# Kernel optimization log

Hardware: AMD Instinct MI355X
Metric: run time of the kernel (lower is better)

## Reference

```python
import jax, jax.numpy as jnp
import numpy as np

B, L, E, H, Dff = 2, 2048, 1024, 16, 4096
Dh = E // H


def _ln(x, g, b, eps=1e-5):
    m = jnp.mean(x, axis=-1, keepdims=True)
    v = jnp.mean((x - m) ** 2, axis=-1, keepdims=True)
    return (x - m) / jnp.sqrt(v + eps) * g + b


def setup_inputs() -> dict:
    key = jax.random.key(0)
    ks = jax.random.split(key, 16)
    s_e = 1.0 / np.sqrt(E)
    s_d = 1.0 / np.sqrt(Dff)
    inp = {
        "x": jax.random.normal(ks[0], (B, L, E), jnp.float32),
        # causal mask: positions with 0 are masked out (masked_fill(mask==0, -1e9))
        "mask": jnp.tril(jnp.ones((L, L), jnp.bool_)),
        # per-head QKV projections, stacked over heads: (H, E, Dh), biases (H, Dh)
        "Wq": jax.random.uniform(ks[1], (H, E, Dh), jnp.float32, -s_e, s_e),
        "bq": jax.random.uniform(ks[2], (H, Dh), jnp.float32, -s_e, s_e),
        "Wk": jax.random.uniform(ks[3], (H, E, Dh), jnp.float32, -s_e, s_e),
        "bk": jax.random.uniform(ks[4], (H, Dh), jnp.float32, -s_e, s_e),
        "Wv": jax.random.uniform(ks[5], (H, E, Dh), jnp.float32, -s_e, s_e),
        "bv": jax.random.uniform(ks[6], (H, Dh), jnp.float32, -s_e, s_e),
        "Wo": jax.random.uniform(ks[7], (E, E), jnp.float32, -s_e, s_e),
        "bo": jax.random.uniform(ks[8], (E,), jnp.float32, -s_e, s_e),
        "W1": jax.random.uniform(ks[9], (E, Dff), jnp.float32, -s_e, s_e),
        "c1": jax.random.uniform(ks[10], (Dff,), jnp.float32, -s_e, s_e),
        "W2": jax.random.uniform(ks[11], (Dff, E), jnp.float32, -s_d, s_d),
        "c2": jax.random.uniform(ks[12], (E,), jnp.float32, -s_d, s_d),
        "g1": jnp.ones((E,), jnp.float32),
        "beta1": jnp.zeros((E,), jnp.float32),
        "g2": jnp.ones((E,), jnp.float32),
        "beta2": jnp.zeros((E,), jnp.float32),
    }
    return inp


def reference(x, mask, Wq, bq, Wk, bk, Wv, bv, Wo, bo, W1, c1, W2, c2, g1, beta1, g2, beta2):
    # Batched equivalent of the per-head Attention loop (eval mode: dropout = identity)
    q = jnp.einsum("ble,hed->bhld", x, Wq) + bq[None, :, None, :]
    k = jnp.einsum("ble,hed->bhld", x, Wk) + bk[None, :, None, :]
    v = jnp.einsum("ble,hed->bhld", x, Wv) + bv[None, :, None, :]
    scores = jnp.einsum("bhld,bhmd->bhlm", q, k) / np.sqrt(Dh).astype(np.float32)
    scores = jnp.where(mask[None, None, :, :], scores, -1e9)
    p = jax.nn.softmax(scores, axis=-1)
    z = jnp.einsum("bhlm,bhmd->bhld", p, v)  # (B,H,L,Dh)
    z = z.transpose(0, 2, 1, 3).reshape(B, L, E)  # concat heads
    att = z @ Wo + bo
    h = _ln(x + att, g1, beta1)
    ff = jax.nn.relu(h @ W1 + c1) @ W2 + c2
    out = _ln(h + ff, g2, beta2)
    return out
```

## Files before the change

kernel.cpp:

```cpp
#include <hip/hip_runtime.h>
#include <hip/hip_bf16.h>
#include <math.h>

#define B_   2
#define L_   2048
#define E_   1024
#define H_   16
#define DH   64
#define DFF  4096
#define M_   4096
#define APAD 72
#define SCALE_Q 0.18033688011112042f

typedef __attribute__((ext_vector_type(8))) short short8;
typedef __attribute__((ext_vector_type(4))) float f32x4;
typedef __bf16 bf16x8 __attribute__((ext_vector_type(8)));

__device__ __forceinline__ float bf2f(unsigned short u) {
    return __uint_as_float(((unsigned)u) << 16);
}
__device__ __forceinline__ unsigned short f2bf(float f) {
    unsigned u = __float_as_uint(f);
    return (unsigned short)((u + 0x7fff + ((u >> 16) & 1)) >> 16);
}
__device__ __forceinline__ unsigned pk_trunc(float lo, float hi) {
    return (__float_as_uint(lo) >> 16) | (__float_as_uint(hi) & 0xffff0000u);
}

__device__ __forceinline__ void gld16(const unsigned short* g, unsigned short* l) {
    __builtin_amdgcn_global_load_lds(
        (const __attribute__((address_space(1))) void*)g,
        (__attribute__((address_space(3))) void*)l, 16, 0, 0);
}

__global__ __launch_bounds__(256) void prep(const float* __restrict__ x,
                                            const float* __restrict__ Wq,
                                            const float* __restrict__ Wk,
                                            const float* __restrict__ Wv,
                                            const float* __restrict__ bq,
                                            const float* __restrict__ bk,
                                            const float* __restrict__ bv,
                                            const float* __restrict__ Wo,
                                            const float* __restrict__ W1,
                                            const float* __restrict__ W2,
                                            unsigned short* __restrict__ xb,
                                            unsigned short* __restrict__ Wqkvt,
                                            unsigned short* __restrict__ Wot,
                                            unsigned short* __restrict__ W1t,
                                            unsigned short* __restrict__ W2t,
                                            float* __restrict__ bqkv) {
    __shared__ float tile[32][33];
    int bid = blockIdx.x;
    const int t = threadIdx.x;

    if (bid < 4096) {
        int i = (bid * 256 + t) * 4;
        float4 v = *(const float4*)&x[i];
        ushort4 pk = { f2bf(v.x), f2bf(v.y), f2bf(v.z), f2bf(v.w) };
        *(ushort4*)&xb[i] = pk;
        return;
    }
    bid -= 4096;

    const float* in; unsigned short* outp; int R, C, r0, c0; float sc = 1.f;
    if (bid < 3072) {
        int xq = bid & 1, yq = (bid >> 1) & 31, wh = bid >> 6;
        int which = wh >> 4, h = wh & 15;
        in   = (which == 0 ? Wq : which == 1 ? Wk : Wv) + (size_t)h * E_ * DH;
        outp = Wqkvt + ((size_t)which * 1024 + h * 64) * 1024;
        R = E_; C = DH; r0 = yq * 32; c0 = xq * 32;
        if (which == 0) sc = SCALE_Q;
    } else if (bid < 4096) {
        bid -= 3072;
        in = Wo; outp = Wot; R = E_; C = E_;
        c0 = (bid & 31) * 32; r0 = (bid >> 5) * 32;
    } else if (bid < 8192) {
        bid -= 4096;
        in = W1; outp = W1t; R = E_; C = DFF;
        c0 = (bid & 127) * 32; r0 = (bid >> 7) * 32;
    } else if (bid < 12288) {
        bid -= 8192;
        in = W2; outp = W2t; R = DFF; C = E_;
        c0 = (bid & 31) * 32; r0 = (bid >> 5) * 32;
    } else {
        bid -= 12288;
        int n = bid * 256 + t;
        bqkv[n] = n < 1024 ? bq[n] * SCALE_Q : n < 2048 ? bk[n - 1024] : bv[n - 2048];
        return;
    }

    const int tx = t & 31, tq = t >> 5;
#pragma unroll
    for (int s2 = 0; s2 < 4; s2++)
        tile[tq * 4 + s2][tx] = in[(size_t)(r0 + tq * 4 + s2) * C + c0 + tx] * sc;
    __syncthreads();
    const int cc = t >> 3, rq = (t & 7) * 4;
    ushort4 pk = { f2bf(tile[rq + 0][cc]), f2bf(tile[rq + 1][cc]),
                   f2bf(tile[rq + 2][cc]), f2bf(tile[rq + 3][cc]) };
    *(ushort4*)&outp[(size_t)(c0 + cc) * R + r0 + rq] = pk;
}

__global__ __launch_bounds__(256) void v_transpose_perm(const unsigned short* __restrict__ qkv,
                                                        unsigned short* __restrict__ vtg) {
    __shared__ unsigned short tile[64 * APAD];
    const int t  = threadIdx.x;
    const int kt = blockIdx.x, hh = blockIdx.y, b = blockIdx.z;
    const int rr0 = t >> 3, o8 = (t & 7) * 8, rr1 = rr0 + 32;
    const size_t gbase = ((size_t)b * L_ + kt * 64) * 3072 + 2048 + hh * 64;
    *(short8*)&tile[rr0 * APAD + o8] = *(const short8*)&qkv[gbase + (size_t)rr0 * 3072 + o8];
    *(short8*)&tile[rr1 * APAD + o8] = *(const short8*)&qkv[gbase + (size_t)rr1 * 3072 + o8];
    __syncthreads();
    const size_t obase = ((size_t)(b * H_ + hh) * 64) * (size_t)L_ + kt * 64;
    const int a = t & 15, d0 = (t >> 4) * 4;
#pragma unroll
    for (int s2 = 0; s2 < 4; s2++) {
        int d = d0 + s2;
        ushort4 pk = { tile[(a +  0) * APAD + d], tile[(a + 16) * APAD + d],
                       tile[(a + 32) * APAD + d], tile[(a + 48) * APAD + d] };
        *(ushort4*)&vtg[obase + (size_t)d * L_ + 4 * a] = pk;
    }
}

#define BAR() __builtin_amdgcn_s_barrier()
#define PIN() __builtin_amdgcn_sched_barrier(0)

#define RD_A(DST, BB, QR) do {                                                \
    _Pragma("unroll") for (int mi = 0; mi < 4; mi++)                          \
    _Pragma("unroll") for (int ks = 0; ks < 2; ks++)                          \
        DST[mi][ks] = *(const bf16x8*)&As[(BB) * 16384 + ((QR) * 128 + aRow + mi * 16) * 64 + (ks ? cs1 : cs0)]; \
} while (0)

#define RD_B(DST, BB, QC) do {                                                \
    _Pragma("unroll") for (int nj = 0; nj < 2; nj++)                          \
    _Pragma("unroll") for (int ks = 0; ks < 2; ks++)                          \
        DST[nj][ks] = *(const bf16x8*)&Bs[(BB) * 16384 + ((QC) * 128 + bRow + nj * 16) * 64 + (ks ? cs1 : cs0)]; \
} while (0)

#define MM(QR, QC, AF, BF) do {                                               \
    __builtin_amdgcn_s_setprio(1);                                            \
    _Pragma("unroll") for (int mi = 0; mi < 4; mi++)                          \
    _Pragma("unroll") for (int nj = 0; nj < 2; nj++)                          \
    _Pragma("unroll") for (int ks = 0; ks < 2; ks++)                          \
        acc[QR][QC][mi][nj] = __builtin_amdgcn_mfma_f32_16x16x32_bf16(        \
            AF[mi][ks], BF[nj][ks], acc[QR][QC][mi][nj], 0, 0, 0);            \
    __builtin_amdgcn_s_setprio(0);                                            \
} while (0)

template <int RELU, int SK>
__global__ __launch_bounds__(512, 2) void gemm256(const unsigned short* __restrict__ A,
                                                  const unsigned short* __restrict__ Bt,
                                                  const float* __restrict__ bias,
                                                  unsigned short* __restrict__ P0,
                                                  unsigned short* __restrict__ P1,
                                                  unsigned short* __restrict__ P2,
                                                  unsigned short* __restrict__ P3,
                                                  int M, int N, int K) {
    extern __shared__ __align__(16) unsigned short g_lds[];
    unsigned short* As = g_lds;
    unsigned short* Bs = g_lds + 32768;

    const int t    = threadIdx.x;
    const int lane = t & 63;
    const int w    = t >> 6;
    const int quad = lane >> 4;
    const int l16  = lane & 15;

    const int lin = blockIdx.x;
    const int xcd = lin & 7, s = lin >> 3;
    int m0, n0, kbeg, KT;
    unsigned short* C;
    if (SK) {
        m0 = ((xcd << 1) | (s & 1)) * 256;
        const int rest = s >> 1;
        n0 = (rest & 3) * 256;
        const int z  = rest >> 2;
        const int K4 = K >> 2;
        kbeg = z * K4;
        KT   = K4 >> 6;
        C = (z == 0) ? P0 : (z == 1) ? P1 : (z == 2) ? P2 : P3;
    } else {
        const int NT2 = (N >> 8) >> 1;
        m0 = (((xcd & 3) << 2) | (s & 3)) * 256;
        n0 = ((xcd >> 2) * NT2 + (s >> 2)) * 256;
        kbeg = 0;
        KT   = K >> 6;
        C = P0;
    }

    const int srow = t >> 3;
    const int ksw  = ((t & 7) ^ (srow & 7)) * 8;
    const size_t aStage = (size_t)(m0 + srow) * K + kbeg + ksw;
    const size_t bStage = (size_t)(n0 + srow) * K + kbeg + ksw;

    auto stageA = [&](int buf, int h, int v) {
        size_t g = aStage + (size_t)(h * 128) * K + (size_t)v * 64;
        unsigned short* l = As + buf * 16384 + h * 8192 + w * 512;
        gld16(A + g, l);
        gld16(A + g + (size_t)64 * K, l + 4096);
    };
    auto stageB = [&](int buf, int h, int v) {
        size_t g = bStage + (size_t)(h * 128) * K + (size_t)v * 64;
        unsigned short* l = Bs + buf * 16384 + h * 8192 + w * 512;
        gld16(Bt + g, l);
        gld16(Bt + g + (size_t)64 * K, l + 4096);
    };

    const int aRow = (w >> 2) * 64 + l16;
    const int bRow = (w & 3) * 32 + l16;
    const int cs0  = (quad ^ (l16 & 7)) * 8;
    const int cs1  = cs0 ^ 32;

    f32x4 acc[2][2][4][2];
#pragma unroll
    for (int a1i = 0; a1i < 2; a1i++)
#pragma unroll
        for (int a2 = 0; a2 < 2; a2++)
#pragma unroll
            for (int a3 = 0; a3 < 4; a3++)
#pragma unroll
                for (int a4 = 0; a4 < 2; a4++)
                    acc[a1i][a2][a3][a4] = (f32x4){0.f, 0.f, 0.f, 0.f};

    bf16x8 a0[4][2], a1[4][2], b0[2][2], b1[2][2];

    stageA(0, 0, 0); stageB(0, 0, 0); stageA(0, 1, 0); stageB(0, 1, 0);
    if (KT > 1) {
        stageA(1, 0, 1); stageB(1, 0, 1);
        asm volatile("s_waitcnt vmcnt(4)" ::: "memory");
    } else {
        asm volatile("s_waitcnt vmcnt(0)" ::: "memory");
    }
    BAR();
    RD_A(a0, 0, 0);
    RD_B(b0, 0, 0);
    PIN();

    for (int u = 0; u < KT; ++u) {
        const int bb = u & 1;
        const int nb = bb ^ 1;

        RD_B(b1, bb, 1);
        if (u + 1 < KT) stageB(nb, 1, u + 1);
        PIN();
        BAR();
        MM(0, 0, a0, b0);
        BAR();

        RD_A(a1, bb, 1);
        if (u + 1 < KT) stageA(nb, 1, u + 1);
        PIN();
        BAR();
        MM(0, 1, a0, b1);
        BAR();

        if (u + 2 < KT) stageA(bb, 0, u + 2);
        PIN();
        BAR();
        MM(1, 0, a1, b0);
        BAR();

        if (u + 2 < KT) {
            stageB(bb, 0, u + 2);
            asm volatile("s_waitcnt vmcnt(4)" ::: "memory");
        } else if (u + 1 < KT) {
            asm volatile("s_waitcnt vmcnt(0)" ::: "memory");
        }
        PIN();
        BAR();
        if (u + 1 < KT) {
            RD_A(a0, nb, 0);
            RD_B(b0, nb, 0);
            PIN();
        }
        MM(1, 1, a1, b1);
        BAR();
    }

#pragma unroll
    for (int qr = 0; qr < 2; qr++)
#pragma unroll
        for (int qc = 0; qc < 2; qc++)
#pragma unroll
            for (int nj = 0; nj < 2; nj++) {
                const int col = n0 + qc * 128 + (w & 3) * 32 + nj * 16 + l16;
                const float bv = SK ? 0.f : bias[col];
#pragma unroll
                for (int mi = 0; mi < 4; mi++) {
                    const int row = m0 + qr * 128 + (w >> 2) * 64 + mi * 16 + quad * 4;
#pragma unroll
                    for (int r = 0; r < 4; r++) {
                        float v = acc[qr][qc][mi][nj][r] + bv;
                        if (RELU) v = fmaxf(v, 0.f);
                        C[(size_t)(row + r) * N + col] = f2bf(v);
                    }
                }
            }
}

__global__ __launch_bounds__(256, 2) void attn_mfma(const unsigned short* __restrict__ qkv,
                                                    const unsigned short* __restrict__ vtg,
                                                    unsigned short* __restrict__ oA,
                                                    unsigned short* __restrict__ oB,
                                                    float* __restrict__ lA,
                                                    float* __restrict__ lB) {
    __shared__ __align__(16) unsigned short ks[2][64 * APAD];
    __shared__ __align__(16) unsigned short vt[64 * APAD];
    __shared__ __align__(16) unsigned short ps[128 * APAD];

    const int t    = threadIdx.x;
    const int lane = t & 63;
    const int w    = t >> 6;
    const int l16  = lane & 15;
    const int quad = lane >> 4;

    const int lin  = blockIdx.x;
    const int unit = lin >> 8;
    const int l8   = lin & 255;
    const int xcd  = l8 & 7;
    const int s    = l8 >> 3;
    const int hh   = xcd * 2 + (s & 1);
    const int rest = s >> 1;
    const int b    = rest & 1;
    const int pair = rest >> 1;

    unsigned short* __restrict__ oP = unit ? oB : oA;
    float* __restrict__ lP = unit ? lB : lA;

    const size_t rowbase = (size_t)b * L_;
    const size_t vbase   = ((size_t)(b * H_ + hh) * 64) * (size_t)L_;
    const int rr0 = t >> 3, o8 = (t & 7) * 8, rr1 = rr0 + 32;

    for (int ph = 0; ph < 2; ph++) {
        const int qq = ph ? pair : 15 - pair;
        const int cnt = qq + 1;

        bf16x8 qf[2][2];
#pragma unroll
        for (int g = 0; g < 2; g++) {
            size_t qrow = rowbase + qq * 128 + w * 32 + g * 16 + l16;
#pragma unroll
            for (int c = 0; c < 2; c++)
                qf[g][c] = *(const bf16x8*)&qkv[qrow * 3072 + hh * 64 + c * 32 + quad * 8];
        }

        f32x4 o[2][4];
#pragma unroll
        for (int g = 0; g < 2; g++)
#pragma unroll
            for (int j = 0; j < 4; j++) o[g][j] = (f32x4){0.f, 0.f, 0.f, 0.f};
        float l_i[2][4] = {};

        {
            size_t kg = (rowbase + unit * 64) * 3072 + 1024 + hh * 64;
            short8 k0 = *(const short8*)&qkv[kg + (size_t)rr0 * 3072 + o8];
            short8 k1 = *(const short8*)&qkv[kg + (size_t)rr1 * 3072 + o8];
            short8 v0 = *(const short8*)&vtg[vbase + unit * 64 + (size_t)rr0 * L_ + o8];
            short8 v1 = *(const short8*)&vtg[vbase + unit * 64 + (size_t)rr1 * L_ + o8];
            *(short8*)&ks[0][rr0 * APAD + o8] = k0;
            *(short8*)&ks[0][rr1 * APAD + o8] = k1;
            *(short8*)&vt[rr0 * APAD + o8] = v0;
            *(short8*)&vt[rr1 * APAD + o8] = v1;
        }

        short8 k0a, k0b, v0a, v0b, k1a, k1b, v1a, v1b;
        if (cnt > 1) {
            const int kt1 = unit + 2;
            size_t kg = (rowbase + kt1 * 64) * 3072 + 1024 + hh * 64;
            k1a = *(const short8*)&qkv[kg + (size_t)rr0 * 3072 + o8];
            k1b = *(const short8*)&qkv[kg + (size_t)rr1 * 3072 + o8];
            size_t vg = vbase + kt1 * 64;
            v1a = *(const short8*)&vtg[vg + (size_t)rr0 * L_ + o8];
            v1b = *(const short8*)&vtg[vg + (size_t)rr1 * L_ + o8];
        }

        auto tile_body = [&](int i,
                             short8& ika, short8& ikb, short8& iva, short8& ivb,
                             short8& wka, short8& wkb, short8& wva, short8& wvb) {
            const int kt = unit + 2 * i;
            const int p  = i & 1;
            __syncthreads();

            if (i + 2 < cnt) {
                size_t kg = (rowbase + (kt + 4) * 64) * 3072 + 1024 + hh * 64;
                ika = *(const short8*)&qkv[kg + (size_t)rr0 * 3072 + o8];
                ikb = *(const short8*)&qkv[kg + (size_t)rr1 * 3072 + o8];
                size_t vg = vbase + (kt + 4) * 64;
                iva = *(const short8*)&vtg[vg + (size_t)rr0 * L_ + o8];
                ivb = *(const short8*)&vtg[vg + (size_t)rr1 * L_ + o8];
            }

            f32x4 s4[2][4];
#pragma unroll
            for (int g = 0; g < 2; g++)
#pragma unroll
                for (int j = 0; j < 4; j++) s4[g][j] = (f32x4){0.f, 0.f, 0.f, 0.f};
            __builtin_amdgcn_s_setprio(1);
#pragma unroll
            for (int c = 0; c < 2; c++)
#pragma unroll
                for (int j = 0; j < 4; j++) {
                    bf16x8 kf = *(const bf16x8*)&ks[p][(j * 16 + l16) * APAD + c * 32 + quad * 8];
#pragma unroll
                    for (int g = 0; g < 2; g++)
                        s4[g][j] = __builtin_amdgcn_mfma_f32_16x16x32_bf16(qf[g][c], kf, s4[g][j], 0, 0, 0);
                }
            __builtin_amdgcn_s_setprio(0);

            if (kt >= 2 * qq) {
#pragma unroll
                for (int g = 0; g < 2; g++)
#pragma unroll
                    for (int j = 0; j < 4; j++) {
                        int lk = kt * 64 + j * 16 + l16;
#pragma unroll
                        for (int r = 0; r < 4; r++)
                            if (lk > qq * 128 + w * 32 + g * 16 + quad * 4 + r)
                                s4[g][j][r] = -INFINITY;
                    }
            }

#pragma unroll
            for (int g = 0; g < 2; g++)
#pragma unroll
                for (int r = 0; r < 4; r++) {
                    float p0 = __builtin_amdgcn_exp2f(s4[g][0][r]);
                    float p1 = __builtin_amdgcn_exp2f(s4[g][1][r]);
                    float p2 = __builtin_amdgcn_exp2f(s4[g][2][r]);
                    float p3 = __builtin_amdgcn_exp2f(s4[g][3][r]);
                    l_i[g][r] += (p0 + p1) + (p2 + p3);
                    uint2 pk = { pk_trunc(p0, p1), pk_trunc(p2, p3) };
                    *(uint2*)&ps[(w * 32 + g * 16 + quad * 4 + r) * APAD + 4 * l16] = pk;
                }

            __builtin_amdgcn_s_waitcnt(0xc07f);

            __builtin_amdgcn_s_setprio(1);
#pragma unroll
            for (int c = 0; c < 2; c++) {
                bf16x8 pf[2];
#pragma unroll
                for (int g = 0; g < 2; g++)
                    pf[g] = *(const bf16x8*)&ps[(w * 32 + g * 16 + l16) * APAD + c * 32 + quad * 8];
#pragma unroll
                for (int j = 0; j < 4; j++) {
                    bf16x8 vf = *(const bf16x8*)&vt[(j * 16 + l16) * APAD + c * 32 + quad * 8];
#pragma unroll
                    for (int g = 0; g < 2; g++)
                        o[g][j] = __builtin_amdgcn_mfma_f32_16x16x32_bf16(pf[g], vf, o[g][j], 0, 0, 0);
                }
            }
            __builtin_amdgcn_s_setprio(0);

            __syncthreads();
            if (i + 1 < cnt) {
                *(short8*)&ks[p ^ 1][rr0 * APAD + o8] = wka;
                *(short8*)&ks[p ^ 1][rr1 * APAD + o8] = wkb;
                *(short8*)&vt[rr0 * APAD + o8] = wva;
                *(short8*)&vt[rr1 * APAD + o8] = wvb;
            }
        };

        for (int i = 0; i < cnt; i += 2) {
            tile_body(i,     k0a, k0b, v0a, v0b, k1a, k1b, v1a, v1b);
            if (i + 1 < cnt)
                tile_body(i + 1, k1a, k1b, v1a, v1b, k0a, k0b, v0a, v0b);
        }

#pragma unroll
        for (int g = 0; g < 2; g++)
#pragma unroll
            for (int r = 0; r < 4; r++) {
                float l = l_i[g][r];
                l += __shfl_xor(l, 1);
                l += __shfl_xor(l, 2);
                l += __shfl_xor(l, 4);
                l += __shfl_xor(l, 8);
                int rowq = qq * 128 + w * 32 + g * 16 + quad * 4 + r;
                size_t grow = (size_t)(b * H_ + hh) * L_ + rowq;
                if (l16 == 0) lP[grow] = l;
#pragma unroll
                for (int j = 0; j < 4; j++)
                    oP[grow * 64 + j * 16 + l16] = f2bf(o[g][j][r]);
            }
    }
}

__global__ __launch_bounds__(256) void attn_combine(const unsigned short* __restrict__ oA,
                                                    const unsigned short* __restrict__ oB,
                                                    const float* __restrict__ lA,
                                                    const float* __restrict__ lB,
                                                    unsigned short* __restrict__ zb) {
    const int t = threadIdx.x;
    const size_t idx4 = ((size_t)blockIdx.x * 256 + t) * 4;
    const size_t row  = idx4 >> 6;
    const int    col  = (int)(idx4 & 63);

    float inv = 1.f / (lA[row] + lB[row]);
    ushort4 ua = *(const ushort4*)&oA[idx4];
    ushort4 ub = *(const ushort4*)&oB[idx4];

    const int bq   = (int)(row >> 15);
    const int hh   = (int)((row >> 11) & 15);
    const int rowq = (int)(row & 2047);
    size_t z = ((size_t)(bq * L_ + rowq)) * 1024 + hh * 64 + col;
    ushort4 pk = { f2bf((bf2f(ua.x) + bf2f(ub.x)) * inv),
                   f2bf((bf2f(ua.y) + bf2f(ub.y)) * inv),
                   f2bf((bf2f(ua.z) + bf2f(ub.z)) * inv),
                   f2bf((bf2f(ua.w) + bf2f(ub.w)) * inv) };
    *(ushort4*)&zb[z] = pk;
}

template <int WRITE_BF16>
__global__ __launch_bounds__(256) void ln5_kernel(const float* __restrict__ a,
                                                  const unsigned short* __restrict__ q0,
                                                  const unsigned short* __restrict__ q1,
                                                  const unsigned short* __restrict__ q2,
                                                  const unsigned short* __restrict__ q3,
                                                  const float* __restrict__ bias,
                                                  const float* __restrict__ g,
                                                  const float* __restrict__ be,
                                                  float* __restrict__ out,
                                                  unsigned short* __restrict__ out_bf) {
    __shared__ float s1[256], s2[256];
    const int row = blockIdx.x;
    const int t   = threadIdx.x;
    const size_t base = (size_t)row * E_ + t * 4;

    float4 ya = *(const float4*)&a[base];
    ushort4 u0 = *(const ushort4*)&q0[base];
    ushort4 u1 = *(const ushort4*)&q1[base];
    ushort4 u2 = *(const ushort4*)&q2[base];
    ushort4 u3 = *(const ushort4*)&q3[base];
    float4 bb = *(const float4*)&bias[t * 4];
    float y0 = ya.x + bb.x + bf2f(u0.x) + bf2f(u1.x) + bf2f(u2.x) + bf2f(u3.x);
    float y1 = ya.y + bb.y + bf2f(u0.y) + bf2f(u1.y) + bf2f(u2.y) + bf2f(u3.y);
    float y2 = ya.z + bb.z + bf2f(u0.z) + bf2f(u1.z) + bf2f(u2.z) + bf2f(u3.z);
    float y3 = ya.w + bb.w + bf2f(u0.w) + bf2f(u1.w) + bf2f(u2.w) + bf2f(u3.w);

    s1[t] = y0 + y1 + y2 + y3;
    s2[t] = y0 * y0 + y1 * y1 + y2 * y2 + y3 * y3;
    __syncthreads();
    for (int off = 128; off > 0; off >>= 1) {
        if (t < off) { s1[t] += s1[t + off]; s2[t] += s2[t + off]; }
        __syncthreads();
    }
    float mean = s1[0] * (1.0f / E_);
    float var  = s2[0] * (1.0f / E_) - mean * mean;
    float rstd = rsqrtf(var + 1e-5f);

    float4 gv = *(const float4*)&g[t * 4];
    float4 bv = *(const float4*)&be[t * 4];
    float4 ov;
    ov.x = (y0 - mean) * rstd * gv.x + bv.x;
    ov.y = (y1 - mean) * rstd * gv.y + bv.y;
    ov.z = (y2 - mean) * rstd * gv.z + bv.z;
    ov.w = (y3 - mean) * rstd * gv.w + bv.w;
    *(float4*)&out[base] = ov;
    if (WRITE_BF16) {
        ushort4 pk = { f2bf(ov.x), f2bf(ov.y), f2bf(ov.z), f2bf(ov.w) };
        *(ushort4*)&out_bf[base] = pk;
    }
}

extern "C" void kernel_launch(void* const* d_in, const int* in_sizes, int n_in,
                              void* d_out, int out_size, void* d_ws, size_t ws_size,
                              hipStream_t stream)
{
    const float* x     = (const float*)d_in[0];
    const float* Wq    = (const float*)d_in[2];
    const float* bq    = (const float*)d_in[3];
    const float* Wk    = (const float*)d_in[4];
    const float* bk    = (const float*)d_in[5];
    const float* Wv    = (const float*)d_in[6];
    const float* bv    = (const float*)d_in[7];
    const float* Wo    = (const float*)d_in[8];
    const float* bo    = (const float*)d_in[9];
    const float* W1    = (const float*)d_in[10];
    const float* c1    = (const float*)d_in[11];
    const float* W2    = (const float*)d_in[12];
    const float* c2    = (const float*)d_in[13];
    const float* g1    = (const float*)d_in[14];
    const float* beta1 = (const float*)d_in[15];
    const float* g2    = (const float*)d_in[16];
    const float* beta2 = (const float*)d_in[17];
    float* out = (float*)d_out;

    const size_t MB = 1024 * 1024;
    char* w = (char*)d_ws;
    unsigned short* xb    = (unsigned short*)(w + 0 * MB);
    unsigned short* Wqkvt = (unsigned short*)(w + 8 * MB);
    unsigned short* Wot   = (unsigned short*)(w + 14 * MB);
    unsigned short* W1t   = (unsigned short*)(w + 16 * MB);
    unsigned short* W2t   = (unsigned short*)(w + 24 * MB);
    float*          bqkv  = (float*)(w + 32 * MB);
    unsigned short* qkv   = (unsigned short*)(w + 33 * MB);
    float*          h     = (float*)(w + 65 * MB);
    unsigned short* vtg   = (unsigned short*)(w + 89 * MB);
    unsigned short* oPA   = (unsigned short*)(w + 57 * MB);
    unsigned short* oPB   = (unsigned short*)(w + 81 * MB);
    float*          lPA   = (float*)(w + 32 * MB);
    float*          lPB   = (float*)(w + 32 * MB + 262144);
    unsigned short* zb    = (unsigned short*)(w + 0 * MB);
    unsigned short* ap0   = (unsigned short*)(w + 33 * MB);
    unsigned short* ap1   = (unsigned short*)(w + 41 * MB);
    unsigned short* ap2   = (unsigned short*)(w + 49 * MB);
    unsigned short* ap3   = (unsigned short*)(w + 89 * MB);
    unsigned short* hb    = (unsigned short*)(w + 0 * MB);
    unsigned short* ff1b  = (unsigned short*)(w + 33 * MB);
    unsigned short* fp0   = (unsigned short*)(w + 0 * MB);
    unsigned short* fp1   = (unsigned short*)(w + 8 * MB);
    unsigned short* fp2   = (unsigned short*)(w + 16 * MB);
    unsigned short* fp3   = (unsigned short*)(w + 81 * MB);

    static bool lds_inited = false;
    if (!lds_inited) {
        (void)hipFuncSetAttribute((const void*)&gemm256<0, 0>,
                                  hipFuncAttributeMaxDynamicSharedMemorySize, 131072);
        (void)hipFuncSetAttribute((const void*)&gemm256<1, 0>,
                                  hipFuncAttributeMaxDynamicSharedMemorySize, 131072);
        (void)hipFuncSetAttribute((const void*)&gemm256<0, 1>,
                                  hipFuncAttributeMaxDynamicSharedMemorySize, 131072);
        lds_inited = true;
    }

    dim3 blk(256);
    dim3 blk2(512);

    prep<<<dim3(16396), blk, 0, stream>>>(x, Wq, Wk, Wv, bq, bk, bv, Wo, W1, W2,
                                          xb, Wqkvt, Wot, W1t, W2t, bqkv);

    gemm256<0, 0><<<dim3(192), blk2, 131072, stream>>>(xb, Wqkvt, bqkv,
                                                       qkv, nullptr, nullptr, nullptr,
                                                       M_, 3072, E_);

    v_transpose_perm<<<dim3(L_ / 64, H_, B_), blk, 0, stream>>>(qkv, vtg);

    attn_mfma<<<dim3(512), blk, 0, stream>>>(qkv, vtg, oPA, oPB, lPA, lPB);

    attn_combine<<<dim3(4096), blk, 0, stream>>>(oPA, oPB, lPA, lPB, zb);

    gemm256<0, 1><<<dim3(256), blk2, 131072, stream>>>(zb, Wot, nullptr,
                                                       ap0, ap1, ap2, ap3,
                                                       M_, E_, E_);

    ln5_kernel<1><<<dim3(M_), blk, 0, stream>>>(x, ap0, ap1, ap2, ap3, bo, g1, beta1, h, hb);

    gemm256<1, 0><<<dim3(256), blk2, 131072, stream>>>(hb, W1t, c1,
                                                       ff1b, nullptr, nullptr, nullptr,
                                                       M_, DFF, E_);

    gemm256<0, 1><<<dim3(256), blk2, 131072, stream>>>(ff1b, W2t, nullptr,
                                                       fp0, fp1, fp2, fp3,
                                                       M_, E_, DFF);

    ln5_kernel<0><<<dim3(M_), blk, 0, stream>>>(h, fp0, fp1, fp2, fp3, c2, g2, beta2, out, nullptr);
}
```

Before: 333.9 us.

## Fuse attention split-combine into the output-projection GEMM A-tile staging

Removes the separate attn_combine kernel and instead has the Wo split-K GEMM build its A tiles by loading both partial attention outputs and their row sums, normalizing, and writing bf16 into LDS. This drops one launch and the write and re-read of the combined z buffer. In exchange, A staging now goes through registers rather than direct global-to-LDS loads, with extra waitcnt on LDS writes, which may weaken the software pipeline. Each split-K block does a single 64-wide head slice per k-step.

```diff
diff --git a/kernel.cpp b/kernel.cpp
--- a/kernel.cpp
+++ b/kernel.cpp
@@ -31,6 +31,16 @@
     __builtin_amdgcn_global_load_lds(
         (const __attribute__((address_space(1))) void*)g,
         (__attribute__((address_space(3))) void*)l, 16, 0, 0);
+}
+
+__device__ __forceinline__ short8 comb8(short8 a, short8 b, float inv) {
+    short8 r;
+#pragma unroll
+    for (int i = 0; i < 8; i++) {
+        float v = (bf2f((unsigned short)a[i]) + bf2f((unsigned short)b[i])) * inv;
+        r[i] = (short)f2bf(v);
+    }
+    return r;
 }
 
 __global__ __launch_bounds__(256) void prep(const float* __restrict__ x,
@@ -146,7 +156,7 @@
     __builtin_amdgcn_s_setprio(0);                                            \
 } while (0)
 
-template <int RELU, int SK>
+template <int RELU, int SK, int COMB>
 __global__ __launch_bounds__(512, 2) void gemm256(const unsigned short* __restrict__ A,
                                                   const unsigned short* __restrict__ Bt,
                                                   const float* __restrict__ bias,
@@ -154,6 +164,10 @@
                                                   unsigned short* __restrict__ P1,
                                                   unsigned short* __restrict__ P2,
                                                   unsigned short* __restrict__ P3,
+                                                  const unsigned short* __restrict__ oAp,
+                                                  const unsigned short* __restrict__ oBp,
+                                                  const float* __restrict__ lAp,
+                                                  const float* __restrict__ lBp,
                                                   int M, int N, int K) {
     extern __shared__ __align__(16) unsigned short g_lds[];
     unsigned short* As = g_lds;
@@ -193,10 +207,25 @@
     const size_t bStage = (size_t)(n0 + srow) * K + kbeg + ksw;
 
     auto stageA = [&](int buf, int h, int v) {
-        size_t g = aStage + (size_t)(h * 128) * K + (size_t)v * 64;
-        unsigned short* l = As + buf * 16384 + h * 8192 + w * 512;
-        gld16(A + g, l);
-        gld16(A + g + (size_t)64 * K, l + 4096);
+        if (COMB) {
+            const int head = (kbeg + v * 64) >> 6;
+#pragma unroll
+            for (int hf = 0; hf < 2; hf++) {
+                const int row = m0 + srow + h * 128 + hf * 64;
+                const int tok = row & 2047, bq = row >> 11;
+                const size_t grow = ((size_t)(bq * H_ + head)) * (size_t)L_ + tok;
+                short8 ua = *(const short8*)&oAp[grow * 64 + ksw];
+                short8 ub = *(const short8*)&oBp[grow * 64 + ksw];
+                float inv = 1.f / (lAp[grow] + lBp[grow]);
+                *(short8*)&As[buf * 16384 + h * 8192 + (srow + hf * 64) * 64 + (t & 7) * 8] =
+                    comb8(ua, ub, inv);
+            }
+        } else {
+            size_t g = aStage + (size_t)(h * 128) * K + (size_t)v * 64;
+            unsigned short* l = As + buf * 16384 + h * 8192 + w * 512;
+            gld16(A + g, l);
+            gld16(A + g + (size_t)64 * K, l + 4096);
+        }
     };
     auto stageB = [&](int buf, int h, int v) {
         size_t g = bStage + (size_t)(h * 128) * K + (size_t)v * 64;
@@ -204,6 +233,13 @@
         gld16(Bt + g, l);
         gld16(Bt + g + (size_t)64 * K, l + 4096);
     };
+    auto waitStage = [&]() {
+        if (COMB) asm volatile("s_waitcnt vmcnt(2) lgkmcnt(0)" ::: "memory");
+        else      asm volatile("s_waitcnt vmcnt(4)" ::: "memory");
+    };
+    auto pubA = [&]() {
+        if (COMB) asm volatile("s_waitcnt lgkmcnt(0)" ::: "memory");
+    };
 
     const int aRow = (w >> 2) * 64 + l16;
     const int bRow = (w & 3) * 32 + l16;
@@ -226,9 +262,9 @@
     stageA(0, 0, 0); stageB(0, 0, 0); stageA(0, 1, 0); stageB(0, 1, 0);
     if (KT > 1) {
         stageA(1, 0, 1); stageB(1, 0, 1);
-        asm volatile("s_waitcnt vmcnt(4)" ::: "memory");
+        waitStage();
     } else {
-        asm volatile("s_waitcnt vmcnt(0)" ::: "memory");
+        asm volatile("s_waitcnt vmcnt(0) lgkmcnt(0)" ::: "memory");
     }
     BAR();
     RD_A(a0, 0, 0);
@@ -248,12 +284,14 @@
 
         RD_A(a1, bb, 1);
         if (u + 1 < KT) stageA(nb, 1, u + 1);
+        pubA();
         PIN();
         BAR();
         MM(0, 1, a0, b1);
         BAR();
 
         if (u + 2 < KT) stageA(bb, 0, u + 2);
+        pubA();
         PIN();
         BAR();
         MM(1, 0, a1, b0);
@@ -261,9 +299,9 @@
 
         if (u + 2 < KT) {
             stageB(bb, 0, u + 2);
-            asm volatile("s_waitcnt vmcnt(4)" ::: "memory");
+            waitStage();
         } else if (u + 1 < KT) {
-            asm volatile("s_waitcnt vmcnt(0)" ::: "memory");
+            asm volatile("s_waitcnt vmcnt(0) lgkmcnt(0)" ::: "memory");
         }
         PIN();
         BAR();
@@ -483,31 +521,6 @@
                     oP[grow * 64 + j * 16 + l16] = f2bf(o[g][j][r]);
             }
     }
-}
-
-__global__ __launch_bounds__(256) void attn_combine(const unsigned short* __restrict__ oA,
-                                                    const unsigned short* __restrict__ oB,
-                                                    const float* __restrict__ lA,
-                                                    const float* __restrict__ lB,
-                                                    unsigned short* __restrict__ zb) {
-    const int t = threadIdx.x;
-    const size_t idx4 = ((size_t)blockIdx.x * 256 + t) * 4;
-    const size_t row  = idx4 >> 6;
-    const int    col  = (int)(idx4 & 63);
-
-    float inv = 1.f / (lA[row] + lB[row]);
-    ushort4 ua = *(const ushort4*)&oA[idx4];
-    ushort4 ub = *(const ushort4*)&oB[idx4];
-
-    const int bq   = (int)(row >> 15);
-    const int hh   = (int)((row >> 11) & 15);
-    const int rowq = (int)(row & 2047);
-    size_t z = ((size_t)(bq * L_ + rowq)) * 1024 + hh * 64 + col;
-    ushort4 pk = { f2bf((bf2f(ua.x) + bf2f(ub.x)) * inv),
-                   f2bf((bf2f(ua.y) + bf2f(ub.y)) * inv),
-                   f2bf((bf2f(ua.z) + bf2f(ub.z)) * inv),
-                   f2bf((bf2f(ua.w) + bf2f(ub.w)) * inv) };
-    *(ushort4*)&zb[z] = pk;
 }
 
 template <int WRITE_BF16>
@@ -600,7 +613,6 @@
     unsigned short* oPB   = (unsigned short*)(w + 81 * MB);
     float*          lPA   = (float*)(w + 32 * MB);
     float*          lPB   = (float*)(w + 32 * MB + 262144);
-    unsigned short* zb    = (unsigned short*)(w + 0 * MB);
     unsigned short* ap0   = (unsigned short*)(w + 33 * MB);
     unsigned short* ap1   = (unsigned short*)(w + 41 * MB);
     unsigned short* ap2   = (unsigned short*)(w + 49 * MB);
@@ -614,11 +626,13 @@
 
     static bool lds_inited = false;
     if (!lds_inited) {
-        (void)hipFuncSetAttribute((const void*)&gemm256<0, 0>,
+        (void)hipFuncSetAttribute((const void*)&gemm256<0, 0, 0>,
                                   hipFuncAttributeMaxDynamicSharedMemorySize, 131072);
-        (void)hipFuncSetAttribute((const void*)&gemm256<1, 0>,
+        (void)hipFuncSetAttribute((const void*)&gemm256<1, 0, 0>,
                                   hipFuncAttributeMaxDynamicSharedMemorySize, 131072);
-        (void)hipFuncSetAttribute((const void*)&gemm256<0, 1>,
+        (void)hipFuncSetAttribute((const void*)&gemm256<0, 1, 0>,
+                                  hipFuncAttributeMaxDynamicSharedMemorySize, 131072);
+        (void)hipFuncSetAttribute((const void*)&gemm256<0, 1, 1>,
                                   hipFuncAttributeMaxDynamicSharedMemorySize, 131072);
         lds_inited = true;
     }
@@ -629,29 +643,31 @@
     prep<<<dim3(16396), blk, 0, stream>>>(x, Wq, Wk, Wv, bq, bk, bv, Wo, W1, W2,
                                           xb, Wqkvt, Wot, W1t, W2t, bqkv);
 
-    gemm256<0, 0><<<dim3(192), blk2, 131072, stream>>>(xb, Wqkvt, bqkv,
-                                                       qkv, nullptr, nullptr, nullptr,
-                                                       M_, 3072, E_);
+    gemm256<0, 0, 0><<<dim3(192), blk2, 131072, stream>>>(xb, Wqkvt, bqkv,
+                                                          qkv, nullptr, nullptr, nullptr,
+                                                          nullptr, nullptr, nullptr, nullptr,
+                                                          M_, 3072, E_);
 
     v_transpose_perm<<<dim3(L_ / 64, H_, B_), blk, 0, stream>>>(qkv, vtg);
 
     attn_mfma<<<dim3(512), blk, 0, stream>>>(qkv, vtg, oPA, oPB, lPA, lPB);
 
-    attn_combine<<<dim3(4096), blk, 0, stream>>>(oPA, oPB, lPA, lPB, zb);
-
-    gemm256<0, 1><<<dim3(256), blk2, 131072, stream>>>(zb, Wot, nullptr,
-                                                       ap0, ap1, ap2, ap3,
-                                                       M_, E_, E_);
+    gemm256<0, 1, 1><<<dim3(256), blk2, 131072, stream>>>(nullptr, Wot, nullptr,
+                                                          ap0, ap1, ap2, ap3,
+                                                          oPA, oPB, lPA, lPB,
+                                                          M_, E_, E_);
 
     ln5_kernel<1><<<dim3(M_), blk, 0, stream>>>(x, ap0, ap1, ap2, ap3, bo, g1, beta1, h, hb);
 
-    gemm256<1, 0><<<dim3(256), blk2, 131072, stream>>>(hb, W1t, c1,
-                                                       ff1b, nullptr, nullptr, nullptr,
-                                                       M_, DFF, E_);
-
-    gemm256<0, 1><<<dim3(256), blk2, 131072, stream>>>(ff1b, W2t, nullptr,
-                                                       fp0, fp1, fp2, fp3,
-                                                       M_, E_, DFF);
+    gemm256<1, 0, 0><<<dim3(256), blk2, 131072, stream>>>(hb, W1t, c1,
+                                                          ff1b, nullptr, nullptr, nullptr,
+                                                          nullptr, nullptr, nullptr, nullptr,
+                                                          M_, DFF, E_);
+
+    gemm256<0, 1, 0><<<dim3(256), blk2, 131072, stream>>>(ff1b, W2t, nullptr,
+                                                          fp0, fp1, fp2, fp3,
+                                                          nullptr, nullptr, nullptr, nullptr,
+                                                          M_, E_, DFF);
 
     ln5_kernel<0><<<dim3(M_), blk, 0, stream>>>(h, fp0, fp1, fp2, fp3, c2, g2, beta2, out, nullptr);
 }
```

Result: slower. 344.3 us (+3.1%).
